# Kernel tuning notes

Hardware: AMD Instinct MI355X
Metric: run time of the kernel (lower is better)

The kernel has to match this reference:

```python
import jax, jax.numpy as jnp
import numpy as np

B, T, D, NH, C = 64, 256, 768, 12, 7
DH = D // NH

def setup_inputs() -> dict:
    key = jax.random.key(0)
    ks = jax.random.split(key, 8)
    s = 0.02
    H = jax.random.normal(ks[0], (B, T, D), jnp.float32)
    num_turns = jax.random.randint(ks[1], (B,), 1, T + 1)  # >=1 real turn each
    Wq = jax.random.normal(ks[2], (D, D), jnp.float32) * s
    Wk = jax.random.normal(ks[3], (D, D), jnp.float32) * s
    Wv = jax.random.normal(ks[4], (D, D), jnp.float32) * s
    Wo = jax.random.normal(ks[5], (D, D), jnp.float32) * s
    Wc = jax.random.normal(ks[6], (2 * D, C), jnp.float32) * s
    bq = jnp.zeros((D,), jnp.float32); bk = jnp.zeros((D,), jnp.float32)
    bv = jnp.zeros((D,), jnp.float32); bo = jnp.zeros((D,), jnp.float32)
    bc = jnp.zeros((C,), jnp.float32)
    return dict(H=H, Wq=Wq, bq=bq, Wk=Wk, bk=bk, Wv=Wv, bv=bv, Wo=Wo, bo=bo,
                Wc=Wc, bc=bc, num_turns=num_turns)

def reference(H, Wq, bq, Wk, bk, Wv, bv, Wo, bo, Wc, bc, num_turns):
    # Vectorized form of the per-(dialogue, turn) python loop:
    # turn t attends (multi-head) over strictly-earlier real turns.
    q = (H @ Wq + bq).reshape(B, T, NH, DH)
    k = (H @ Wk + bk).reshape(B, T, NH, DH)
    v = (H @ Wv + bv).reshape(B, T, NH, DH)
    scores = jnp.einsum('bqhd,bkhd->bhqk', q, k) / np.sqrt(DH).astype(np.float32)
    tq = jnp.arange(T)
    # strict causal (key < query) AND key is a real (non-padding) turn
    mask = (tq[None, :, None] > tq[None, None, :]) & (tq[None, None, :] < num_turns[:, None, None])  # [B,T,T]
    scores = jnp.where(mask[:, None], scores, -1e30)
    attn = jax.nn.softmax(scores, axis=-1)
    row_valid = mask.any(-1)  # [B,T]; False for t=0 (and beyond padding prefix logic)
    attn = jnp.where(row_valid[:, None, :, None], attn, 0.0)
    ctx = jnp.einsum('bhqk,bkhd->bqhd', attn, v).reshape(B, T, D)
    c = ctx @ Wo + bo
    # t==0: original sets c_t = exact zeros (no out-proj bias) -> zero full rows
    c = jnp.where(row_valid[:, :, None], c, 0.0)
    z = jnp.concatenate([H, c], axis=-1)          # [B,T,2D]
    all_logits = z @ Wc + bc                       # [B,T,C]
    final_logits = all_logits[jnp.arange(B), num_turns - 1]  # [B,C]
    return all_logits, final_logits
```

## Files before the change

### kernel.cpp

```cpp
#include <hip/hip_runtime.h>
#include <hip/hip_bf16.h>

#define B_  64
#define T_  256
#define D_  768
#define NH_ 12
#define DH_ 64
#define C_  7
#define QS_ 2304

using f32x4  = __attribute__((ext_vector_type(4))) float;
using bf16x8 = __attribute__((ext_vector_type(8))) __bf16;
using u16x8  = __attribute__((ext_vector_type(8))) unsigned short;
using u16x4  = __attribute__((ext_vector_type(4))) unsigned short;
using s16x4  = __attribute__((ext_vector_type(4))) short;

#if defined(__has_builtin)
#if __has_builtin(__builtin_amdgcn_mfma_f32_16x16x16bf16_1k)
#define HAS_MFMA16 1
#endif
#endif

static __device__ inline unsigned short f2bf(float f) {
    union { float f; unsigned u; } c; c.f = f;
    unsigned u = c.u;
    return (unsigned short)((u + 0x7fffu + ((u >> 16) & 1u)) >> 16);
}

#define ASYNC16(gp, lp) __builtin_amdgcn_global_load_lds(                      \
    (const __attribute__((address_space(1))) unsigned int*)(gp),               \
    (__attribute__((address_space(3))) unsigned int*)(lp), 16, 0, 0)

#define PRO_CONV 6144
#define PRO_TR   1728
#define PRO_BIAS 9
#define PRO_WF   13
#define PRO_ALL  (PRO_CONV + PRO_TR + PRO_BIAS + PRO_WF)

__global__ __launch_bounds__(256) void prologue(
    const float* __restrict__ H, unsigned short* __restrict__ Hb,
    const float* __restrict__ Wq, const float* __restrict__ Wk,
    const float* __restrict__ Wv,
    unsigned short* __restrict__ Wqkvt,
    const float* __restrict__ bq, const float* __restrict__ bk,
    const float* __restrict__ bv, float* __restrict__ bqkv,
    const float* __restrict__ Wo, const float* __restrict__ Wc,
    const float* __restrict__ bo,
    float* __restrict__ Wf, float* __restrict__ boc)
{
    __shared__ float tile[32][33];
    __shared__ float wcs[D_ * C_];
    const int blk = blockIdx.x;
    const int tid = threadIdx.x;

    if (blk < PRO_CONV) {
        const int i = (blk * 256 + tid) * 8;
        float4 f0 = *(const float4*)(H + i);
        float4 f1 = *(const float4*)(H + i + 4);
        u16x8 u;
        u[0] = f2bf(f0.x); u[1] = f2bf(f0.y); u[2] = f2bf(f0.z); u[3] = f2bf(f0.w);
        u[4] = f2bf(f1.x); u[5] = f2bf(f1.y); u[6] = f2bf(f1.z); u[7] = f2bf(f1.w);
        *(uint4*)(Hb + i) = __builtin_bit_cast(uint4, u);
    } else if (blk < PRO_CONV + PRO_TR) {
        const int tb = blk - PRO_CONV;
        const int z = tb / 576;
        const int rem = tb - z * 576;
        const int bx = (rem % 24) * 32;
        const int by = (rem / 24) * 32;
        const size_t wsz = (size_t)D_ * D_;
        const float* W = (z == 0) ? Wq : (z == 1) ? Wk : Wv;
        unsigned short* Wt = Wqkvt + (size_t)z * wsz;
        const int tx = tid & 31;
        const int ty = tid >> 5;
#pragma unroll
        for (int i = ty; i < 32; i += 8)
            tile[i][tx] = W[(size_t)(by + i) * D_ + bx + tx];
        __syncthreads();
#pragma unroll
        for (int i = ty; i < 32; i += 8)
            Wt[(size_t)(bx + i) * D_ + by + tx] = f2bf(tile[tx][i]);
    } else if (blk < PRO_CONV + PRO_TR + PRO_BIAS) {
        const int i = (blk - PRO_CONV - PRO_TR) * 256 + tid;
        if (i < D_)          bqkv[i] = bq[i];
        else if (i < 2 * D_) bqkv[i] = bk[i - D_];
        else if (i < 3 * D_) bqkv[i] = bv[i - 2 * D_];
    } else {
        const int fb = blk - (PRO_CONV + PRO_TR + PRO_BIAS);
        for (int i = tid; i < D_ * C_; i += 256)
            wcs[i] = Wc[(size_t)D_ * C_ + i];
        __syncthreads();
        if (fb < 12) {
            const int dl = tid >> 2;
            const int ks = tid & 3;
            const int d  = fb * 64 + dl;
            const float* wrow = Wo + (size_t)d * D_;
            float a[C_] = {};
            for (int e = ks * 192; e < ks * 192 + 192; ++e) {
                const float w = wrow[e];
#pragma unroll
                for (int c = 0; c < C_; ++c) a[c] += w * wcs[e * C_ + c];
            }
#pragma unroll
            for (int c = 0; c < C_; ++c) {
                a[c] += __shfl_xor(a[c], 1, 64);
                a[c] += __shfl_xor(a[c], 2, 64);
            }
            if (ks == 0) {
#pragma unroll
                for (int c = 0; c < C_; ++c) Wf[d * C_ + c] = a[c];
            }
        } else if (tid < C_) {
            float a = 0.f;
            for (int e = 0; e < D_; ++e) a += bo[e] * wcs[e * C_ + tid];
            boc[tid] = a;
        }
    }
}

#define QBM 128
#define QBN 256
#define QBK 64
#define KQ  768
#define NKT 12

#define BAR   __builtin_amdgcn_s_barrier()
#define LGKM0 do { asm volatile("s_waitcnt lgkmcnt(0)" ::: "memory");          \
                   __builtin_amdgcn_sched_barrier(0); } while (0)
#define VMW(n) do { asm volatile("s_waitcnt vmcnt(" #n ")" ::: "memory");      \
                    __builtin_amdgcn_sched_barrier(0); } while (0)

__global__ __launch_bounds__(512, 2) void gemm_qkv_8ph(
    const unsigned short* __restrict__ A,
    const unsigned short* __restrict__ Bt,
    const float* __restrict__ bias,
    unsigned short* __restrict__ qkvb,
    unsigned short* __restrict__ Vt,
    const int* __restrict__ num_turns)
{
    __shared__ unsigned short As[3][QBM * QBK];
    __shared__ unsigned short Bs[3][QBN * QBK];

    const int tid = threadIdx.x;
    const int wid = tid >> 6;
    const int ln  = tid & 63;
    const int hi  = ln >> 4;
    const int lo  = ln & 15;
    const int wm  = (wid >> 2) * 64;
    const int wn  = (wid & 3) * 64;

    const int L   = blockIdx.y * gridDim.x + blockIdx.x;
    const int xcd = L & 7;
    const int li  = L >> 3;
    const int wg  = xcd * 144 + li;
    const int my  = wg / 9;
    const int nx  = wg - my * 9;

    const int row0 = my * QBM;
    const int col0 = nx * QBN;

    if (col0 >= D_ && (row0 & (T_ - 1)) != 0) {
        if (num_turns[row0 >> 8] <= 128) return;
    }

    const int s0 = tid >> 3;
    const int ch = (tid & 7) ^ (s0 & 7);
    const unsigned short* a0 = A  + (size_t)(row0 + s0) * KQ + ch * 8;
    const unsigned short* b0 = Bt + (size_t)(col0 + s0) * KQ + ch * 8;

#define STG_A(t, q) do {                                                       \
    ASYNC16(a0 + (size_t)(t) * QBK,                &As[q][       wid * 512]);  \
    ASYNC16(a0 + (size_t)(t) * QBK +  64 * KQ,     &As[q][4096 + wid * 512]);  \
} while (0)
#define STG_B(t, q) do {                                                       \
    ASYNC16(b0 + (size_t)(t) * QBK,                &Bs[q][        wid * 512]); \
    ASYNC16(b0 + (size_t)(t) * QBK +  64 * KQ,     &Bs[q][ 4096 + wid * 512]); \
    ASYNC16(b0 + (size_t)(t) * QBK + 128 * KQ,     &Bs[q][ 8192 + wid * 512]); \
    ASYNC16(b0 + (size_t)(t) * QBK + 192 * KQ,     &Bs[q][12288 + wid * 512]); \
} while (0)

    const int fcs[2] = { (0 * 4 + hi) ^ (lo & 7), (1 * 4 + hi) ^ (lo & 7) };

    f32x4  acc[4][4] = {};
    bf16x8 af[4][2];
    bf16x8 bA[2][2];
    bf16x8 bBa[2][2], bBb[2][2], bBc[2][2];

    STG_B(0, 0); STG_A(0, 0); STG_B(1, 1); STG_A(1, 1); STG_B(2, 2);
    VMW(10); BAR;

#define GROUP(gg, q, qa, BW, BR) do {                                          \
    if ((gg) + 2 < NKT) STG_A((gg) + 2, qa);                                   \
    _Pragma("unroll") for (int nf = 0; nf < 2; ++nf)                           \
    _Pragma("unroll") for (int ks = 0; ks < 2; ++ks) {                         \
        bA[nf][ks] = *(const bf16x8*)&Bs[q][(wn + nf * 16 + lo) * QBK + fcs[ks] * 8];       \
        BW[nf][ks] = *(const bf16x8*)&Bs[q][(wn + (nf + 2) * 16 + lo) * QBK + fcs[ks] * 8]; \
    }                                                                          \
    if ((gg) != 0) {                                                           \
        __builtin_amdgcn_s_setprio(1);                                         \
        _Pragma("unroll") for (int mf = 0; mf < 4; ++mf)                       \
        _Pragma("unroll") for (int nf = 0; nf < 2; ++nf)                       \
        _Pragma("unroll") for (int ks = 0; ks < 2; ++ks)                       \
            acc[mf][nf + 2] = __builtin_amdgcn_mfma_f32_16x16x32_bf16(         \
                af[mf][ks], BR[nf][ks], acc[mf][nf + 2], 0, 0, 0);             \
        __builtin_amdgcn_s_setprio(0);                                         \
    }                                                                          \
    LGKM0; BAR;                                                                \
    if ((gg) + 3 < NKT) STG_B((gg) + 3, q);                                    \
    _Pragma("unroll") for (int mf = 0; mf < 4; ++mf)                           \
    _Pragma("unroll") for (int ks = 0; ks < 2; ++ks)                           \
        af[mf][ks] = *(const bf16x8*)&As[q][(wm + mf * 16 + lo) * QBK + fcs[ks] * 8]; \
    __builtin_amdgcn_s_setprio(1);                                             \
    _Pragma("unroll") for (int mf = 0; mf < 4; ++mf)                           \
    _Pragma("unroll") for (int nf = 0; nf < 2; ++nf)                           \
    _Pragma("unroll") for (int ks = 0; ks < 2; ++ks)                           \
        acc[mf][nf] = __builtin_amdgcn_mfma_f32_16x16x32_bf16(                 \
            af[mf][ks], bA[nf][ks], acc[mf][nf], 0, 0, 0);                     \
    __builtin_amdgcn_s_setprio(0);                                             \
    if ((gg) + 1 < NKT) {                                                      \
        if ((gg) + 3 < NKT)      VMW(10);                                      \
        else if ((gg) + 2 < NKT) VMW(6);                                       \
        else                     VMW(0);                                       \
    }                                                                          \
    LGKM0; BAR;                                                                \
} while (0)

    for (int g = 0; g < NKT; g += 3) {
        GROUP(g + 0, 0, 2, bBa, bBc);
        GROUP(g + 1, 1, 0, bBb, bBa);
        GROUP(g + 2, 2, 1, bBc, bBb);
    }

    __builtin_amdgcn_s_setprio(1);
#pragma unroll
    for (int mf = 0; mf < 4; ++mf)
#pragma unroll
        for (int nf = 0; nf < 2; ++nf)
#pragma unroll
            for (int ks = 0; ks < 2; ++ks)
                acc[mf][nf + 2] = __builtin_amdgcn_mfma_f32_16x16x32_bf16(
                    af[mf][ks], bBc[nf][ks], acc[mf][nf + 2], 0, 0, 0);
    __builtin_amdgcn_s_setprio(0);

    const int bidx = row0 >> 8;
    const int t0   = row0 & (T_ - 1);
    if (col0 >= 1536) {
#pragma unroll
        for (int j = 0; j < 4; ++j) {
            const int dcol = (col0 - 1536) + wn + j * 16 + lo;
            const float bcol = bias[col0 + wn + j * 16 + lo];
            unsigned short* vrow =
                Vt + ((size_t)(bidx * NH_ + (dcol >> 6)) * DH_ + (dcol & 63)) * T_ + t0;
#pragma unroll
            for (int i = 0; i < 4; ++i) {
                u16x4 pk;
#pragma unroll
                for (int r = 0; r < 4; ++r) pk[r] = f2bf(acc[i][j][r] + bcol);
                *(u16x4*)(vrow + wm + i * 16 + hi * 4) = pk;
            }
        }
        return;
    }
#pragma unroll
    for (int j = 0; j < 4; ++j) {
        const int col = col0 + wn + j * 16 + lo;
        const float bcol = bias[col];
#pragma unroll
        for (int i = 0; i < 4; ++i) {
#pragma unroll
            for (int r = 0; r < 4; ++r) {
                const int row = row0 + wm + i * 16 + hi * 4 + r;
                qkvb[(size_t)row * QS_ + col] = f2bf(acc[i][j][r] + bcol);
            }
        }
    }
#undef STG_A
#undef STG_B
#undef GROUP
}

#if HAS_MFMA16
__global__ __launch_bounds__(512) void attn_fused(
    const unsigned short* __restrict__ qkv, const unsigned short* __restrict__ Vt,
    const int* __restrict__ num_turns, unsigned short* __restrict__ ctx)
{
    __shared__ unsigned short Klds[256 * 64];
    __shared__ unsigned short Vlds[64 * 256];

    const int bh = blockIdx.x;
    const int b = bh / NH_;
    const int h = bh - b * NH_;
    const int tid = threadIdx.x;
    const int wave = tid >> 6;
    const int lane = tid & 63;
    const int hi = lane >> 4;
    const int lo = lane & 15;
    const int lo7 = lo & 7;

    const int nt = num_turns[b];
    const int kend16 = (min(254, nt - 1) >> 4) + 1;
    const int vst = (kend16 <= 8) ? 128 : 256;

    const unsigned short* qb  = qkv + (size_t)(b * T_) * QS_ + h * DH_;
    const unsigned short* kb  = qb + D_;
    const unsigned short* vtb = Vt + (size_t)bh * DH_ * T_;

    {
        const int nkc = kend16 * 128;
        for (int q = tid; q < nkc; q += 512) {
            const int row = q >> 3;
            const int c   = q & 7;
            const int sl  = c ^ (row & 7);
            uint4 v = *(const uint4*)(kb + (size_t)row * QS_ + c * 8);
            *(uint4*)&Klds[row * 64 + sl * 8] = v;
        }
    }
    if (vst == 256) {
        for (int q = tid; q < 2048; q += 512) {
            const int d  = q >> 5;
            const int c  = q & 31;
            const int sl = c ^ (d & 7);
            uint4 v = *(const uint4*)(vtb + (size_t)d * T_ + c * 8);
            *(uint4*)&Vlds[d * 256 + sl * 8] = v;
        }
    } else {
        for (int q = tid; q < 1024; q += 512) {
            const int d  = q >> 4;
            const int c  = q & 15;
            const int sl = c ^ (d & 7);
            uint4 v = *(const uint4*)(vtb + (size_t)d * T_ + c * 8);
            *(uint4*)&Vlds[d * 128 + sl * 8] = v;
        }
    }

    bf16x8 aqs[2][2];
#pragma unroll
    for (int i = 0; i < 2; ++i) {
        const int m0 = (i ? (15 - wave) : wave) * 16;
#pragma unroll
        for (int ks = 0; ks < 2; ++ks)
            aqs[i][ks] = *(const bf16x8*)(qb + (size_t)(m0 + lo) * QS_ + ks * 32 + hi * 8);
    }

    __syncthreads();

#pragma unroll
    for (int i = 0; i < 2; ++i) {
        const int tq = i ? (15 - wave) : wave;
        const int m0 = tq * 16;
        const int qrow = m0 + lo;
        const int kmax  = min(m0 + 14, nt - 1);
        const int ktmax = kmax >> 4;

        f32x4 s[16] = {};
#pragma unroll
        for (int kt = 0; kt < 16; ++kt) {
            if (kt <= ktmax) {
#pragma unroll
                for (int ks = 0; ks < 2; ++ks) {
                    bf16x8 kf = *(const bf16x8*)&Klds[(kt * 16 + lo) * 64
                                                     + ((ks * 4 + hi) ^ lo7) * 8];
                    s[kt] = __builtin_amdgcn_mfma_f32_16x16x32_bf16(kf, aqs[i][ks], s[kt], 0, 0, 0);
                }
            }
        }

        float lsum = 0.f;
        s16x4 pf[16];
#pragma unroll
        for (int kt = 0; kt < 16; ++kt) {
            if (kt <= ktmax) {
#pragma unroll
                for (int r = 0; r < 4; ++r) {
                    const int key = kt * 16 + hi * 4 + r;
                    const bool valid = (key < qrow) && (key < nt);
                    const float p = valid ? __expf(s[kt][r] * 0.125f) : 0.f;
                    lsum += p;
                    pf[kt][r] = (short)f2bf(p);
                }
            }
        }

        f32x4 o[4] = {};
#pragma unroll
        for (int kt = 0; kt < 16; ++kt) {
            if (kt <= ktmax) {
#pragma unroll
                for (int nd = 0; nd < 4; ++nd) {
                    const int cidx = (kt * 2 + (hi >> 1)) ^ lo7;
                    s16x4 bv = *(const s16x4*)&Vlds[(nd * 16 + lo) * vst
                                                    + cidx * 8 + (hi & 1) * 4];
                    o[nd] = __builtin_amdgcn_mfma_f32_16x16x16bf16_1k(pf[kt], bv, o[nd], 0, 0, 0);
                }
            }
        }

        lsum += __shfl_xor(lsum, 16, 64);
        lsum += __shfl_xor(lsum, 32, 64);
        float linv[4];
#pragma unroll
        for (int r = 0; r < 4; ++r) {
            const float lq = __shfl(lsum, hi * 4 + r, 64);
            linv[r] = (lq > 0.f) ? (1.f / lq) : 0.f;
        }

#pragma unroll
        for (int nd = 0; nd < 4; ++nd) {
#pragma unroll
            for (int r = 0; r < 4; ++r) {
                ctx[((size_t)(b * T_ + m0 + hi * 4 + r)) * D_ + h * DH_ + nd * 16 + lo]
                    = f2bf(o[nd][r] * linv[r]);
            }
        }
    }
}
#else
__global__ __launch_bounds__(512) void attn_fused(
    const unsigned short* __restrict__ qkv, const unsigned short* __restrict__ Vt,
    const int* __restrict__ num_turns, unsigned short* __restrict__ ctx)
{
    __shared__ unsigned short Plds[8][16 * 264];

    const int bh = blockIdx.x;
    const int b = bh / NH_;
    const int h = bh - b * NH_;
    const int tid = threadIdx.x;
    const int wave = tid >> 6;
    const int lane = tid & 63;
    const int hi = lane >> 4;
    const int lo = lane & 15;

    const int nt = num_turns[b];
    const unsigned short* qb = qkv + (size_t)(b * T_) * QS_ + h * DH_;
    const unsigned short* kb = qb + D_;
    const unsigned short* vtb = Vt + (size_t)bh * DH_ * T_;

    for (int ii = 0; ii < 2; ++ii) {
        const int m0 = (ii ? (15 - wave) : wave) * 16;
        const int kmax = min(m0 + 14, nt - 1);
        const int n0hi = (kmax >> 4) | 1;
        const int nks  = (kmax >> 5) + 1;

        bf16x8 aq[2];
#pragma unroll
        for (int ks = 0; ks < 2; ++ks)
            aq[ks] = *(const bf16x8*)(qb + (size_t)(m0 + lo) * QS_ + ks * 32 + hi * 8);

        f32x4 s[16] = {};
#pragma unroll
        for (int n0 = 0; n0 < 16; ++n0) {
            if (n0 <= n0hi) {
#pragma unroll
                for (int ks = 0; ks < 2; ++ks) {
                    bf16x8 bk = *(const bf16x8*)(kb + (size_t)(n0 * 16 + lo) * QS_ + ks * 32 + hi * 8);
                    s[n0] = __builtin_amdgcn_mfma_f32_16x16x32_bf16(aq[ks], bk, s[n0], 0, 0, 0);
                }
            }
        }

#pragma unroll
        for (int r = 0; r < 4; ++r) {
            const int qrow = m0 + hi * 4 + r;
            float mr = -1e30f;
#pragma unroll
            for (int n0 = 0; n0 < 16; ++n0) {
                if (n0 <= n0hi) {
                    int key = n0 * 16 + lo;
                    bool valid = (key < qrow) && (key < nt);
                    float se = valid ? s[n0][r] * 0.125f : -1e30f;
                    s[n0][r] = se;
                    mr = fmaxf(mr, se);
                }
            }
#pragma unroll
            for (int off = 1; off < 16; off <<= 1) mr = fmaxf(mr, __shfl_xor(mr, off, 64));

            float lr = 0.f;
#pragma unroll
            for (int n0 = 0; n0 < 16; ++n0) {
                if (n0 <= n0hi) {
                    float se = s[n0][r];
                    float pv = (se > -5e29f) ? __expf(se - mr) : 0.f;
                    s[n0][r] = pv;
                    lr += pv;
                }
            }
#pragma unroll
            for (int off = 1; off < 16; off <<= 1) lr += __shfl_xor(lr, off, 64);

            float inv = (lr > 0.f) ? (1.f / lr) : 0.f;
#pragma unroll
            for (int n0 = 0; n0 < 16; ++n0) {
                if (n0 <= n0hi) {
                    Plds[wave][(hi * 4 + r) * 264 + n0 * 16 + lo] = f2bf(s[n0][r] * inv);
                }
            }
        }

        f32x4 o[4] = {};
#pragma unroll
        for (int ks = 0; ks < 8; ++ks) {
            if (ks < nks) {
                const unsigned short* lp = &Plds[wave][lo * 264 + ks * 32 + hi * 8];
                bf16x8 ap = __builtin_bit_cast(bf16x8, *(const uint4*)lp);
#pragma unroll
                for (int nd = 0; nd < 4; ++nd) {
                    bf16x8 bvf = *(const bf16x8*)(vtb + (size_t)(nd * 16 + lo) * T_ + ks * 32 + hi * 8);
                    o[nd] = __builtin_amdgcn_mfma_f32_16x16x32_bf16(ap, bvf, o[nd], 0, 0, 0);
                }
            }
        }

#pragma unroll
        for (int nd = 0; nd < 4; ++nd) {
#pragma unroll
            for (int r = 0; r < 4; ++r) {
                ctx[((size_t)(b * T_ + m0 + hi * 4 + r)) * D_ + h * DH_ + nd * 16 + lo]
                    = f2bf(o[nd][r]);
            }
        }
    }
}
#endif

#define WCP 1544

__global__ __launch_bounds__(256) void logits_mfma(
    const unsigned short* __restrict__ Hb, const unsigned short* __restrict__ ctxb,
    const float* __restrict__ Wc, const float* __restrict__ Wf,
    const float* __restrict__ bc, const float* __restrict__ boc,
    const int* __restrict__ num_turns, float* __restrict__ out)
{
    __shared__ unsigned short sW[16 * WCP];

    const int tid = threadIdx.x;
    const int wave = tid >> 6;
    const int lane = tid & 63;
    const int hi = lane >> 4;
    const int lo = lane & 15;

    for (int i = tid; i < 16 * 1536; i += 256) {
        int n = i & 15, kk = i >> 4;
        float val = 0.f;
        if (n < C_)
            val = (kk < D_) ? Wc[(size_t)kk * C_ + n] : Wf[(kk - D_) * C_ + n];
        sW[n * WCP + kk] = f2bf(val);
    }
    __syncthreads();

    const int m0 = blockIdx.x * 64 + wave * 16;
    const unsigned short* hrow = Hb   + (size_t)(m0 + lo) * D_;
    const unsigned short* crow = ctxb + (size_t)(m0 + lo) * D_;

    f32x4 acc = {};
#pragma unroll
    for (int kt = 0; kt < 24; ++kt) {
        bf16x8 a = *(const bf16x8*)(hrow + kt * 32 + hi * 8);
        bf16x8 w = *(const bf16x8*)&sW[lo * WCP + kt * 32 + hi * 8];
        acc = __builtin_amdgcn_mfma_f32_16x16x32_bf16(a, w, acc, 0, 0, 0);
    }
#pragma unroll
    for (int kt = 0; kt < 24; ++kt) {
        bf16x8 a = *(const bf16x8*)(crow + kt * 32 + hi * 8);
        bf16x8 w = *(const bf16x8*)&sW[lo * WCP + (768 + kt * 32) + hi * 8];
        acc = __builtin_amdgcn_mfma_f32_16x16x32_bf16(a, w, acc, 0, 0, 0);
    }

    if (lo < C_) {
        const float b0 = bc[lo];
        const float b1 = boc[lo];
#pragma unroll
        for (int r = 0; r < 4; ++r) {
            const int row = m0 + hi * 4 + r;
            const int t = row & (T_ - 1);
            const float tot = acc[r] + b0 + ((t != 0) ? b1 : 0.f);
            out[(size_t)row * C_ + lo] = tot;
            const int b = row >> 8;
            if (t == num_turns[b] - 1)
                out[(size_t)B_ * T_ * C_ + (size_t)b * C_ + lo] = tot;
        }
    }
}

extern "C" void kernel_launch(void* const* d_in, const int* in_sizes, int n_in,
                              void* d_out, int out_size, void* d_ws, size_t ws_size,
                              hipStream_t stream)
{
    const float* H  = (const float*)d_in[0];
    const float* Wq = (const float*)d_in[1];
    const float* bq = (const float*)d_in[2];
    const float* Wk = (const float*)d_in[3];
    const float* bk = (const float*)d_in[4];
    const float* Wv = (const float*)d_in[5];
    const float* bv = (const float*)d_in[6];
    const float* Wo = (const float*)d_in[7];
    const float* bo = (const float*)d_in[8];
    const float* Wc = (const float*)d_in[9];
    const float* bc = (const float*)d_in[10];
    const int* num_turns = (const int*)d_in[11];
    float* out = (float*)d_out;

    const int M = B_ * T_;
    const size_t per = (size_t)M * D_;
    const size_t wsz = (size_t)D_ * D_;

    unsigned short* ws16 = (unsigned short*)d_ws;
    unsigned short* Hb    = ws16;
    unsigned short* Wqkvt = Hb + per;
    unsigned short* qkvb  = Wqkvt + 3 * wsz;
    unsigned short* ctxb  = qkvb + (size_t)M * QS_;
    unsigned short* Vtb   = ctxb + per;
    float* bqkv = (float*)(Vtb + per);
    float* Wf   = bqkv + QS_;
    float* boc  = Wf + (size_t)D_ * C_;

    prologue<<<PRO_ALL, 256, 0, stream>>>(H, Hb, Wq, Wk, Wv, Wqkvt,
                                          bq, bk, bv, bqkv,
                                          Wo, Wc, bo, Wf, boc);

    dim3 qkvGrid(9, 128);
    gemm_qkv_8ph<<<qkvGrid, 512, 0, stream>>>(Hb, Wqkvt, bqkv, qkvb,
                                              Vtb, num_turns);

    attn_fused<<<B_ * NH_, 512, 0, stream>>>(qkvb, Vtb, num_turns, ctxb);

    logits_mfma<<<M / 64, 256, 0, stream>>>(Hb, ctxb, Wc, Wf, bc, boc,
                                            num_turns, out);
}
```

Measured before the change: 275.6 us.

## Replace triple-buffered 8-phase QKV GEMM with simpler double-buffered 128x128 tile kernel

Drops the 512-thread, 128x256-tile, triple-buffered GEMM with its interleaved A/B staging and split MFMA phases. In its place is a 256-thread, 128x128-tile kernel that double-buffers both operands and runs one stage/wait/barrier/compute step per K tile. The aim is a simpler schedule, less LDS per block and twice as many blocks, which may help occupancy and load balance. The cost is less overlap of global loads with MFMA work and less B-fragment reuse per block.

New measurement: 262.5 us. 1.05x faster.

```diff
diff --git a/kernel.cpp b/kernel.cpp
--- a/kernel.cpp
+++ b/kernel.cpp
@@ -118,18 +118,17 @@
 }
 
 #define QBM 128
-#define QBN 256
+#define QBN 128
 #define QBK 64
 #define KQ  768
 #define NKT 12
 
-#define BAR   __builtin_amdgcn_s_barrier()
-#define LGKM0 do { asm volatile("s_waitcnt lgkmcnt(0)" ::: "memory");          \
+#define BAR   do { __builtin_amdgcn_s_barrier();                               \
                    __builtin_amdgcn_sched_barrier(0); } while (0)
 #define VMW(n) do { asm volatile("s_waitcnt vmcnt(" #n ")" ::: "memory");      \
                     __builtin_amdgcn_sched_barrier(0); } while (0)
 
-__global__ __launch_bounds__(512, 2) void gemm_qkv_8ph(
+__global__ __launch_bounds__(256, 2) void gemm_qkv_db(
     const unsigned short* __restrict__ A,
     const unsigned short* __restrict__ Bt,
     const float* __restrict__ bias,
@@ -137,23 +136,21 @@
     unsigned short* __restrict__ Vt,
     const int* __restrict__ num_turns)
 {
-    __shared__ unsigned short As[3][QBM * QBK];
-    __shared__ unsigned short Bs[3][QBN * QBK];
+    __shared__ unsigned short As[2][QBM * QBK];
+    __shared__ unsigned short Bs[2][QBN * QBK];
 
     const int tid = threadIdx.x;
-    const int wid = tid >> 6;
+    const int wv  = tid >> 6;
     const int ln  = tid & 63;
     const int hi  = ln >> 4;
     const int lo  = ln & 15;
-    const int wm  = (wid >> 2) * 64;
-    const int wn  = (wid & 3) * 64;
+    const int wm  = (wv & 1) * 64;
+    const int wn  = (wv >> 1) * 64;
 
     const int L   = blockIdx.y * gridDim.x + blockIdx.x;
-    const int xcd = L & 7;
-    const int li  = L >> 3;
-    const int wg  = xcd * 144 + li;
-    const int my  = wg / 9;
-    const int nx  = wg - my * 9;
+    const int wg  = (L & 7) * 288 + (L >> 3);
+    const int my  = wg / 18;
+    const int nx  = wg - my * 18;
 
     const int row0 = my * QBM;
     const int col0 = nx * QBN;
@@ -167,79 +164,48 @@
     const unsigned short* a0 = A  + (size_t)(row0 + s0) * KQ + ch * 8;
     const unsigned short* b0 = Bt + (size_t)(col0 + s0) * KQ + ch * 8;
 
-#define STG_A(t, q) do {                                                       \
-    ASYNC16(a0 + (size_t)(t) * QBK,                &As[q][       wid * 512]);  \
-    ASYNC16(a0 + (size_t)(t) * QBK +  64 * KQ,     &As[q][4096 + wid * 512]);  \
+#define STG(t, q) do {                                                         \
+    _Pragma("unroll") for (int c = 0; c < 4; ++c) {                            \
+        ASYNC16(a0 + (size_t)(t) * QBK + (size_t)c * 32 * KQ,                  \
+                &As[q][c * 2048 + wv * 512]);                                  \
+        ASYNC16(b0 + (size_t)(t) * QBK + (size_t)c * 32 * KQ,                  \
+                &Bs[q][c * 2048 + wv * 512]);                                  \
+    }                                                                          \
 } while (0)
-#define STG_B(t, q) do {                                                       \
-    ASYNC16(b0 + (size_t)(t) * QBK,                &Bs[q][        wid * 512]); \
-    ASYNC16(b0 + (size_t)(t) * QBK +  64 * KQ,     &Bs[q][ 4096 + wid * 512]); \
-    ASYNC16(b0 + (size_t)(t) * QBK + 128 * KQ,     &Bs[q][ 8192 + wid * 512]); \
-    ASYNC16(b0 + (size_t)(t) * QBK + 192 * KQ,     &Bs[q][12288 + wid * 512]); \
-} while (0)
 
     const int fcs[2] = { (0 * 4 + hi) ^ (lo & 7), (1 * 4 + hi) ^ (lo & 7) };
 
-    f32x4  acc[4][4] = {};
-    bf16x8 af[4][2];
-    bf16x8 bA[2][2];
-    bf16x8 bBa[2][2], bBb[2][2], bBc[2][2];
-
-    STG_B(0, 0); STG_A(0, 0); STG_B(1, 1); STG_A(1, 1); STG_B(2, 2);
-    VMW(10); BAR;
-
-#define GROUP(gg, q, qa, BW, BR) do {                                          \
-    if ((gg) + 2 < NKT) STG_A((gg) + 2, qa);                                   \
-    _Pragma("unroll") for (int nf = 0; nf < 2; ++nf)                           \
-    _Pragma("unroll") for (int ks = 0; ks < 2; ++ks) {                         \
-        bA[nf][ks] = *(const bf16x8*)&Bs[q][(wn + nf * 16 + lo) * QBK + fcs[ks] * 8];       \
-        BW[nf][ks] = *(const bf16x8*)&Bs[q][(wn + (nf + 2) * 16 + lo) * QBK + fcs[ks] * 8]; \
-    }                                                                          \
-    if ((gg) != 0) {                                                           \
+    f32x4 acc[4][4] = {};
+
+#define TILE(t, q, qn) do {                                                    \
+    if ((t) + 1 < NKT) { STG((t) + 1, qn); VMW(8); }                           \
+    else               { VMW(0); }                                             \
+    BAR;                                                                       \
+    _Pragma("unroll") for (int s = 0; s < 2; ++s) {                            \
+        const int fc = fcs[s];                                                 \
+        bf16x8 af[4], bfr[4];                                                  \
+        _Pragma("unroll") for (int i = 0; i < 4; ++i)                          \
+            af[i] = *(const bf16x8*)&As[q][(wm + i * 16 + lo) * QBK + fc * 8]; \
+        _Pragma("unroll") for (int j = 0; j < 4; ++j)                          \
+            bfr[j] = *(const bf16x8*)&Bs[q][(wn + j * 16 + lo) * QBK + fc * 8];\
         __builtin_amdgcn_s_setprio(1);                                         \
-        _Pragma("unroll") for (int mf = 0; mf < 4; ++mf)                       \
-        _Pragma("unroll") for (int nf = 0; nf < 2; ++nf)                       \
-        _Pragma("unroll") for (int ks = 0; ks < 2; ++ks)                       \
-            acc[mf][nf + 2] = __builtin_amdgcn_mfma_f32_16x16x32_bf16(         \
-                af[mf][ks], BR[nf][ks], acc[mf][nf + 2], 0, 0, 0);             \
+        _Pragma("unroll") for (int i = 0; i < 4; ++i)                          \
+        _Pragma("unroll") for (int j = 0; j < 4; ++j)                          \
+            acc[i][j] = __builtin_amdgcn_mfma_f32_16x16x32_bf16(               \
+                af[i], bfr[j], acc[i][j], 0, 0, 0);                            \
         __builtin_amdgcn_s_setprio(0);                                         \
     }                                                                          \
-    LGKM0; BAR;                                                                \
-    if ((gg) + 3 < NKT) STG_B((gg) + 3, q);                                    \
-    _Pragma("unroll") for (int mf = 0; mf < 4; ++mf)                           \
-    _Pragma("unroll") for (int ks = 0; ks < 2; ++ks)                           \
-        af[mf][ks] = *(const bf16x8*)&As[q][(wm + mf * 16 + lo) * QBK + fcs[ks] * 8]; \
-    __builtin_amdgcn_s_setprio(1);                                             \
-    _Pragma("unroll") for (int mf = 0; mf < 4; ++mf)                           \
-    _Pragma("unroll") for (int nf = 0; nf < 2; ++nf)                           \
-    _Pragma("unroll") for (int ks = 0; ks < 2; ++ks)                           \
-        acc[mf][nf] = __builtin_amdgcn_mfma_f32_16x16x32_bf16(                 \
-            af[mf][ks], bA[nf][ks], acc[mf][nf], 0, 0, 0);                     \
-    __builtin_amdgcn_s_setprio(0);                                             \
-    if ((gg) + 1 < NKT) {                                                      \
-        if ((gg) + 3 < NKT)      VMW(10);                                      \
-        else if ((gg) + 2 < NKT) VMW(6);                                       \
-        else                     VMW(0);                                       \
-    }                                                                          \
-    LGKM0; BAR;                                                                \
+    BAR;                                                                       \
 } while (0)
 
-    for (int g = 0; g < NKT; g += 3) {
-        GROUP(g + 0, 0, 2, bBa, bBc);
-        GROUP(g + 1, 1, 0, bBb, bBa);
-        GROUP(g + 2, 2, 1, bBc, bBb);
-    }
-
-    __builtin_amdgcn_s_setprio(1);
-#pragma unroll
-    for (int mf = 0; mf < 4; ++mf)
-#pragma unroll
-        for (int nf = 0; nf < 2; ++nf)
-#pragma unroll
-            for (int ks = 0; ks < 2; ++ks)
-                acc[mf][nf + 2] = __builtin_amdgcn_mfma_f32_16x16x32_bf16(
-                    af[mf][ks], bBc[nf][ks], acc[mf][nf + 2], 0, 0, 0);
-    __builtin_amdgcn_s_setprio(0);
+    STG(0, 0);
+#pragma unroll
+    for (int g = 0; g < NKT; g += 2) {
+        TILE(g + 0, 0, 1);
+        TILE(g + 1, 1, 0);
+    }
+#undef STG
+#undef TILE
 
     const int bidx = row0 >> 8;
     const int t0   = row0 & (T_ - 1);
@@ -273,9 +239,6 @@
             }
         }
     }
-#undef STG_A
-#undef STG_B
-#undef GROUP
 }
 
 #if HAS_MFMA16
@@ -617,9 +580,9 @@
                                           bq, bk, bv, bqkv,
                                           Wo, Wc, bo, Wf, boc);
 
-    dim3 qkvGrid(9, 128);
-    gemm_qkv_8ph<<<qkvGrid, 512, 0, stream>>>(Hb, Wqkvt, bqkv, qkvb,
-                                              Vtb, num_turns);
+    dim3 qkvGrid(18, 128);
+    gemm_qkv_db<<<qkvGrid, 256, 0, stream>>>(Hb, Wqkvt, bqkv, qkvb,
+                                             Vtb, num_turns);
 
     attn_fused<<<B_ * NH_, 512, 0, stream>>>(qkvb, Vtb, num_turns, ctxb);
 
```
